# Kernel tuning notes

Hardware: AMD Instinct MI355X
Metric: run time of the kernel (lower is better)

The kernel has to match this reference:

```python
import jax, jax.numpy as jnp
import numpy as np

B, N, D, H, K, NH = 4096, 2048, 1024, 4096, 5, 8
HD = D // NH  # head dim


def setup_inputs() -> dict:
    key = jax.random.key(0)
    ks = jax.random.split(key, 12)
    s_d = np.float32(1.0 / np.sqrt(D))
    s_h = np.float32(1.0 / np.sqrt(H))
    rn = lambda k, sh, s: jax.random.normal(k, sh, dtype=jnp.float32) * s
    return {
        "morph0": jax.random.normal(ks[0], (B, D), dtype=jnp.float32),
        "stored_morph0": jax.random.normal(ks[1], (N, D), dtype=jnp.float32),
        "stored_morph1": jax.random.normal(ks[2], (N, D), dtype=jnp.float32),
        "wq": rn(ks[3], (D, D), s_d), "bq": jnp.zeros((D,), jnp.float32),
        "wk": rn(ks[4], (D, D), s_d), "bk": jnp.zeros((D,), jnp.float32),
        "wv": rn(ks[5], (D, D), s_d), "bv": jnp.zeros((D,), jnp.float32),
        "wo": rn(ks[6], (D, D), s_d), "bo": jnp.zeros((D,), jnp.float32),
        "w1": rn(ks[7], (H, D), s_d), "b1": jnp.zeros((H,), jnp.float32),
        "w2": rn(ks[8], (H, H), s_h), "b2": jnp.zeros((H,), jnp.float32),
        "w3": rn(ks[9], (D, H), s_h), "b3": jnp.zeros((D,), jnp.float32),
    }


def _l2norm(x):
    # F.normalize(dim=1): x / max(||x||, eps)
    n = jnp.sqrt(jnp.sum(x * x, axis=-1, keepdims=True))
    return x / jnp.maximum(n, 1e-12)


def reference(morph0, stored_morph0, stored_morph1,
              wq, bq, wk, bk, wv, bv, wo, bo,
              w1, b1, w2, b2, w3, b3):
    # ---- retrieve similar patterns: cosine sim + topk + fused gather-subtract ----
    qn = _l2norm(morph0)                       # [B, D]
    sn = _l2norm(stored_morph0)                # [N, D]
    sim = qn @ sn.T                            # [B, N]
    _, top_idx = jax.lax.top_k(sim, K)         # [B, K]
    evo = stored_morph1 - stored_morph0        # [N, D]
    selected = jnp.take(evo, top_idx, axis=0)  # [B, K, D] evolution vectors

    # ---- torch.nn.MultiheadAttention(D, 8, batch_first=True), eval mode ----
    q = (morph0 @ wq.T + bq).reshape(B, 1, NH, HD)      # [B, 1, NH, HD]
    k = (selected @ wk.T + bk).reshape(B, K, NH, HD)    # [B, K, NH, HD]
    v = (selected @ wv.T + bv).reshape(B, K, NH, HD)
    scores = jnp.einsum('bqhd,bkhd->bhqk', q, k) / np.float32(np.sqrt(HD))  # [B, NH, 1, K]
    attn = jax.nn.softmax(scores, axis=-1)
    ctx = jnp.einsum('bhqk,bkhd->bqhd', attn, v).reshape(B, 1, D)
    context = (ctx @ wo.T + bo)[:, 0, :]                # [B, D]
    attn_weights = attn.mean(axis=1)                    # [B, 1, K] (avg over heads)

    # ---- evolution net (dropout inactive in eval) + residual ----
    x = morph0 + context
    h1 = jax.nn.relu(x @ w1.T + b1)
    h2 = jax.nn.relu(h1 @ w2.T + b2)
    predicted = morph0 + (h2 @ w3.T + b3)
    return predicted, attn_weights
```

## Files before the change

### kernel.cpp

```cpp
#include <hip/hip_runtime.h>
#include <hip/hip_bf16.h>
#include <math.h>

typedef __bf16 bf16_t;
typedef __bf16 bf16x4 __attribute__((ext_vector_type(4)));
typedef __bf16 bf16x8 __attribute__((ext_vector_type(8)));
typedef float  f32x4  __attribute__((ext_vector_type(4)));

#define BB 4096
#define NN 2048
#define DD 1024
#define HH 4096
#define KSEL 5
#define NHEAD 8

__device__ __forceinline__ unsigned short bfbits(float f) {
  return __builtin_bit_cast(unsigned short, (bf16_t)f);
}

__device__ __forceinline__ void gload_lds16(const void* g, void* l) {
  __builtin_amdgcn_global_load_lds(
      (const __attribute__((address_space(1))) void*)g,
      (__attribute__((address_space(3))) void*)l, 16, 0, 0);
}

__device__ __forceinline__ ushort4 cvt4(float4 x) {
  ushort4 o;
  o.x = bfbits(x.x); o.y = bfbits(x.y); o.z = bfbits(x.z); o.w = bfbits(x.w);
  return o;
}

#define P_M0   1048576
#define P_S0   1572864
#define P_EVO  2097152
#define P_WQ   2359296
#define P_WKV  2883584
#define P_WO   3145728
#define P_W1   4194304
#define P_W2   8388608
#define P_W3   9437184
#define P_BKV  9437696
__global__ void __launch_bounds__(256)
prep_k(const float4* __restrict__ m0, const float4* __restrict__ s0,
       const float4* __restrict__ s1,
       const float4* __restrict__ wq, const float4* __restrict__ wk,
       const float4* __restrict__ wv, const float4* __restrict__ wo,
       const float4* __restrict__ w1, const float4* __restrict__ w2,
       const float4* __restrict__ w3,
       const float4* __restrict__ bk, const float4* __restrict__ bv,
       ushort4* __restrict__ m0b, ushort4* __restrict__ s0b,
       ushort4* __restrict__ evo,
       ushort4* __restrict__ wqb, ushort4* __restrict__ wkvb,
       ushort4* __restrict__ wob,
       ushort4* __restrict__ w1b, ushort4* __restrict__ w2b,
       ushort4* __restrict__ w3b, float4* __restrict__ bkv)
{
  const int stride = gridDim.x * 256;
  for (int i = blockIdx.x * 256 + threadIdx.x; i < P_BKV; i += stride) {
    if (i < P_M0) {
      m0b[i] = cvt4(m0[i]);
    } else if (i < P_S0) {
      int j = i - P_M0; s0b[j] = cvt4(s0[j]);
    } else if (i < P_EVO) {
      int j = i - P_S0;
      float4 a = s0[j], b = s1[j];
      float4 d; d.x = b.x - a.x; d.y = b.y - a.y; d.z = b.z - a.z; d.w = b.w - a.w;
      evo[j] = cvt4(d);
    } else if (i < P_WQ) {
      int j = i - P_EVO; wqb[j] = cvt4(wq[j]);
    } else if (i < P_WKV) {
      int j = i - P_WQ;
      wkvb[j] = cvt4(j < 262144 ? wk[j] : wv[j - 262144]);
    } else if (i < P_WO) {
      int j = i - P_WKV; wob[j] = cvt4(wo[j]);
    } else if (i < P_W1) {
      int j = i - P_WO; w1b[j] = cvt4(w1[j]);
    } else if (i < P_W2) {
      int j = i - P_W1; w2b[j] = cvt4(w2[j]);
    } else if (i < P_W3) {
      int j = i - P_W2; w3b[j] = cvt4(w3[j]);
    } else {
      int j = i - P_W3;
      bkv[j] = (j < 256) ? bk[j] : bv[j - 256];
    }
  }
}

__global__ void rnormd_k(const float* __restrict__ s0, double* __restrict__ rnd) {
  __shared__ double red[256];
  int n = blockIdx.x, tid = threadIdx.x;
  const float4* row = (const float4*)(s0 + (size_t)n * DD);
  float4 x = row[tid];
  double ss = (double)x.x * x.x + (double)x.y * x.y + (double)x.z * x.z + (double)x.w * x.w;
  red[tid] = ss; __syncthreads();
  for (int s = 128; s > 0; s >>= 1) {
    if (tid < s) red[tid] += red[tid + s];
    __syncthreads();
  }
  if (tid == 0) rnd[n] = 1.0 / fmax(sqrt(red[0]), 1e-12);
}

template<bool RELU, bool RESID, bool OUTBF16>
__global__ void __launch_bounds__(256)
gemm_bt(const bf16_t* __restrict__ A, const bf16_t* __restrict__ Bw,
        const float* __restrict__ bias, const float* __restrict__ resid,
        float* __restrict__ outf, bf16_t* __restrict__ outb,
        int M, int Nn, int Kk)
{
  __shared__ alignas(16) bf16_t At[2][4096];
  __shared__ alignas(16) bf16_t Bt[2][4096];
  const int tid = threadIdx.x;
  const int wave = tid >> 6, lane = tid & 63;
  const int wm = wave >> 1, wn = wave & 1;
  const int bm = blockIdx.y << 7, bn = blockIdx.x << 7;
  const int ln15 = lane & 15, ln4 = lane >> 4;

  const int srow  = (wave << 4) + (lane >> 2);
  const int scolb = (((lane & 3) ^ ((lane >> 3) & 3)) << 4);
  const char* pA0 = (const char*)A  + (size_t)(bm + srow) * Kk * 2 + scolb;
  const char* pA1 = (const char*)A  + (size_t)(bm + srow + 64) * Kk * 2 + scolb;
  const char* pB0 = (const char*)Bw + (size_t)(bn + srow) * Kk * 2 + scolb;
  const char* pB1 = (const char*)Bw + (size_t)(bn + srow + 64) * Kk * 2 + scolb;

  f32x4 zero = {0.f, 0.f, 0.f, 0.f};
  f32x4 acc[4][4];
  #pragma unroll
  for (int i = 0; i < 4; ++i)
    #pragma unroll
    for (int j = 0; j < 4; ++j) acc[i][j] = zero;

  const int rslot = (ln4 ^ ((ln15 >> 1) & 3)) << 3;
  const int fAoff = ((wm << 6) + ln15) * 32 + rslot;
  const int fBoff = ((wn << 6) + ln15) * 32 + rslot;

  const int nt = Kk >> 5;
  {
    char* lA = (char*)At[0] + (wave << 10);
    char* lB = (char*)Bt[0] + (wave << 10);
    gload_lds16(pA0, lA);
    gload_lds16(pA1, lA + 4096);
    gload_lds16(pB0, lB);
    gload_lds16(pB1, lB + 4096);
  }
  __syncthreads();

  for (int t = 0; t < nt; ++t) {
    const int cur = t & 1;
    if (t + 1 < nt) {
      size_t kb = (size_t)(t + 1) << 6;
      char* lA = (char*)At[cur ^ 1] + (wave << 10);
      char* lB = (char*)Bt[cur ^ 1] + (wave << 10);
      gload_lds16(pA0 + kb, lA);
      gload_lds16(pA1 + kb, lA + 4096);
      gload_lds16(pB0 + kb, lB);
      gload_lds16(pB1 + kb, lB + 4096);
    }
    bf16x8 av[4], bv[4];
    #pragma unroll
    for (int i = 0; i < 4; ++i) av[i] = *(const bf16x8*)(&At[cur][fAoff + i * 512]);
    #pragma unroll
    for (int j = 0; j < 4; ++j) bv[j] = *(const bf16x8*)(&Bt[cur][fBoff + j * 512]);
    #pragma unroll
    for (int i = 0; i < 4; ++i)
      #pragma unroll
      for (int j = 0; j < 4; ++j)
        acc[i][j] = __builtin_amdgcn_mfma_f32_16x16x32_bf16(av[i], bv[j], acc[i][j], 0, 0, 0);
    __syncthreads();
  }

  const int r0 = bm + (wm << 6) + ((lane >> 4) << 2);
  const int c0 = bn + (wn << 6) + ln15;
  #pragma unroll
  for (int i = 0; i < 4; ++i) {
    #pragma unroll
    for (int j = 0; j < 4; ++j) {
      #pragma unroll
      for (int r = 0; r < 4; ++r) {
        int row = r0 + i * 16 + r;
        int col = c0 + j * 16;
        size_t o = (size_t)row * Nn + col;
        float v = acc[i][j][r];
        if (bias)  v += bias[col];
        if (RESID) v += resid[o];
        if (RELU)  v = fmaxf(v, 0.f);
        if (OUTBF16) outb[o] = (bf16_t)v;
        else         outf[o] = v;
      }
    }
  }
}

template<bool RELU>
__global__ void __launch_bounds__(512, 4)
gemm_hp(const bf16_t* __restrict__ A, const bf16_t* __restrict__ Bw,
        const float* __restrict__ bias, bf16_t* __restrict__ outb,
        int Nn, int Kk, int nbx)
{
  __shared__ alignas(16) bf16_t As[2][4096];
  __shared__ alignas(16) bf16_t Bs[2][8192];
  const int tid  = threadIdx.x;
  const int lane = tid & 63, wv = tid >> 6;
  const int wm = wv >> 2, wn = wv & 3;
  const int ln15 = lane & 15, ln4 = lane >> 4;

  const int nwg = gridDim.x;
  const int q = nwg >> 3, r = nwg & 7;
  const int xcd = blockIdx.x & 7, loc = blockIdx.x >> 3;
  const int swz = (xcd < r ? xcd * (q + 1) : r * (q + 1) + (xcd - r) * q) + loc;
  const int bm = (swz / nbx) << 7;
  const int bn = (swz % nbx) << 8;

  const int NT = Kk >> 5;

  f32x4 acc[4][4];
  f32x4 zero = {0.f, 0.f, 0.f, 0.f};
  #pragma unroll
  for (int i = 0; i < 4; ++i)
    #pragma unroll
    for (int j = 0; j < 4; ++j) acc[i][j] = zero;

  const int sslot = (lane & 3) ^ ((lane >> 3) & 3);
  auto stageA = [&](bf16_t* lds, int kt) {
    int row = wv * 16 + (lane >> 2);
    gload_lds16(A + (size_t)(bm + row) * Kk + kt * 32 + sslot * 8,
                (char*)lds + wv * 1024);
  };
  auto stageB = [&](bf16_t* lds, int kt) {
    #pragma unroll
    for (int u = 0; u < 2; ++u) {
      int rowbase = u * 128 + wv * 16;
      int row = rowbase + (lane >> 2);
      gload_lds16(Bw + (size_t)(bn + row) * Kk + kt * 32 + sslot * 8,
                  (char*)lds + rowbase * 64);
    }
  };

  stageA(As[0], 0); stageB(Bs[0], 0);
  asm volatile("s_waitcnt vmcnt(0)" ::: "memory");
  __builtin_amdgcn_s_barrier();
  __builtin_amdgcn_sched_barrier(0);

  const int rslot = (ln4 ^ ((ln15 >> 1) & 3)) << 4;

  for (int t = 0; t < NT; ++t) {
    const int cur = t & 1;
    const char* Ab = (const char*)As[cur];
    const char* Bb = (const char*)Bs[cur];
    const bool more = (t + 1 < NT);
    bf16x8 av[4], bv[4];

    #pragma unroll
    for (int mi = 0; mi < 4; ++mi) {
      const int row = wm * 64 + mi * 16 + ln15;
      av[mi] = *(const bf16x8*)(Ab + row * 64 + rslot);
    }
    #pragma unroll
    for (int nj = 0; nj < 4; ++nj) {
      const int row = wn * 64 + nj * 16 + ln15;
      bv[nj] = *(const bf16x8*)(Bb + row * 64 + rslot);
    }
    if (more) { stageA(As[cur ^ 1], t + 1); stageB(Bs[cur ^ 1], t + 1); }

    __builtin_amdgcn_s_setprio(1);
    #pragma unroll
    for (int mi = 0; mi < 4; ++mi)
      #pragma unroll
      for (int nj = 0; nj < 4; ++nj)
        acc[mi][nj] = __builtin_amdgcn_mfma_f32_16x16x32_bf16(
            av[mi], bv[nj], acc[mi][nj], 0, 0, 0);
    __builtin_amdgcn_s_setprio(0);

    asm volatile("s_waitcnt vmcnt(0)" ::: "memory");
    __builtin_amdgcn_sched_barrier(0);
    __builtin_amdgcn_s_barrier();
    __builtin_amdgcn_sched_barrier(0);
  }

  #pragma unroll
  for (int am = 0; am < 4; ++am) {
    #pragma unroll
    for (int an = 0; an < 4; ++an) {
      #pragma unroll
      for (int rr = 0; rr < 4; ++rr) {
        int row = bm + wm * 64 + am * 16 + (lane >> 4) * 4 + rr;
        int col = bn + wn * 64 + an * 16 + ln15;
        float v = acc[am][an][rr] + bias[col];
        if (RELU) v = fmaxf(v, 0.f);
        outb[(size_t)row * Nn + col] = (bf16_t)v;
      }
    }
  }
}

__global__ void __launch_bounds__(256)
topk8_k(const float* __restrict__ sim, const double* __restrict__ rnd,
        int* __restrict__ cand)
{
  __shared__ float vals[NN];
  __shared__ float rv[256];
  __shared__ int   ri[256];
  int b = blockIdx.x, tid = threadIdx.x;
  for (int t = 0; t < NN / 256; ++t) {
    int i = tid + t * 256;
    vals[i] = sim[(size_t)b * NN + i] * (float)rnd[i];
  }
  __syncthreads();
  for (int p = 0; p < 8; ++p) {
    float bvv = -INFINITY; int bi = NN;
    for (int t = 0; t < NN / 256; ++t) {
      int i = tid + t * 256;
      float v = vals[i];
      if (v > bvv) { bvv = v; bi = i; }
    }
    rv[tid] = bvv; ri[tid] = bi;
    __syncthreads();
    for (int s = 128; s > 0; s >>= 1) {
      if (tid < s) {
        float v2 = rv[tid + s]; int i2 = ri[tid + s];
        if (v2 > rv[tid] || (v2 == rv[tid] && i2 < ri[tid])) { rv[tid] = v2; ri[tid] = i2; }
      }
      __syncthreads();
    }
    if (tid == 0) {
      int wsel = ri[0];
      cand[b * 8 + p] = wsel;
      vals[wsel] = -INFINITY;
    }
    __syncthreads();
  }
}

__global__ void __launch_bounds__(256)
refine_k(const float* __restrict__ m0, const float* __restrict__ s0,
         const double* __restrict__ rnd, const int* __restrict__ cand,
         int* __restrict__ topidx)
{
  __shared__ double red[256];
  __shared__ double vals[8];
  int b = blockIdx.x, tid = threadIdx.x;
  int cs[8];
  #pragma unroll
  for (int j = 0; j < 8; ++j) cs[j] = cand[b * 8 + j];
  const float* q = m0 + (size_t)b * DD;
  double part[8];
  #pragma unroll
  for (int j = 0; j < 8; ++j) part[j] = 0.0;
  for (int d = tid; d < DD; d += 256) {
    double qd = (double)q[d];
    #pragma unroll
    for (int j = 0; j < 8; ++j)
      part[j] += qd * (double)s0[(size_t)cs[j] * DD + d];
  }
  for (int j = 0; j < 8; ++j) {
    red[tid] = part[j]; __syncthreads();
    for (int s = 128; s > 0; s >>= 1) {
      if (tid < s) red[tid] += red[tid + s];
      __syncthreads();
    }
    if (tid == 0) vals[j] = red[0] * rnd[cs[j]];
    __syncthreads();
  }
  if (tid == 0) {
    bool used[8] = {false,false,false,false,false,false,false,false};
    for (int p = 0; p < KSEL; ++p) {
      int best = -1;
      for (int j = 0; j < 8; ++j) {
        if (used[j]) continue;
        if (best < 0 || vals[j] > vals[best] ||
            (vals[j] == vals[best] && cs[j] < cs[best])) best = j;
      }
      used[best] = true;
      topidx[b * KSEL + p] = cs[best];
    }
  }
}

__global__ void __launch_bounds__(256)
attn_k(const bf16_t* __restrict__ q, const bf16_t* __restrict__ eKV,
       const int* __restrict__ tidx,
       bf16_t* __restrict__ ctx, float* __restrict__ attn_out)
{
  __shared__ float aw[NHEAD][KSEL];
  const int b = blockIdx.x, t = threadIdx.x;
  const int d0 = t << 2;
  int idx[KSEL];
  #pragma unroll
  for (int j = 0; j < KSEL; ++j) idx[j] = tidx[b * KSEL + j];

  bf16x4 qv = *(const bf16x4*)(q + (size_t)b * DD + d0);
  float s[KSEL];
  #pragma unroll
  for (int j = 0; j < KSEL; ++j) {
    bf16x4 kv = *(const bf16x4*)(eKV + (size_t)idx[j] * 2048 + d0);
    float p = (float)qv[0] * (float)kv[0] + (float)qv[1] * (float)kv[1]
            + (float)qv[2] * (float)kv[2] + (float)qv[3] * (float)kv[3];
    #pragma unroll
    for (int m = 16; m > 0; m >>= 1) p += __shfl_xor(p, m);
    s[j] = p * 0.08838834764831845f;
  }
  float mx = s[0];
  #pragma unroll
  for (int j = 1; j < KSEL; ++j) mx = fmaxf(mx, s[j]);
  float e[KSEL], sum = 0.f;
  #pragma unroll
  for (int j = 0; j < KSEL; ++j) { e[j] = expf(s[j] - mx); sum += e[j]; }
  float inv = 1.f / sum;

  float c0 = 0.f, c1 = 0.f, c2 = 0.f, c3 = 0.f;
  #pragma unroll
  for (int j = 0; j < KSEL; ++j) {
    float a = e[j] * inv;
    bf16x4 vv = *(const bf16x4*)(eKV + (size_t)idx[j] * 2048 + 1024 + d0);
    c0 += a * (float)vv[0]; c1 += a * (float)vv[1];
    c2 += a * (float)vv[2]; c3 += a * (float)vv[3];
    if ((t & 31) == 0) aw[t >> 5][j] = a;
  }
  bf16x4 co; co[0] = (bf16_t)c0; co[1] = (bf16_t)c1; co[2] = (bf16_t)c2; co[3] = (bf16_t)c3;
  *(bf16x4*)(ctx + (size_t)b * DD + d0) = co;
  __syncthreads();
  if (t < KSEL) {
    float m = 0.f;
    #pragma unroll
    for (int hh = 0; hh < NHEAD; ++hh) m += aw[hh][t];
    attn_out[(size_t)b * KSEL + t] = m * 0.125f;
  }
}

extern "C" void kernel_launch(void* const* d_in, const int* in_sizes, int n_in,
                              void* d_out, int out_size, void* d_ws, size_t ws_size,
                              hipStream_t stream) {
  (void)in_sizes; (void)n_in; (void)out_size; (void)ws_size;
  const float* morph0 = (const float*)d_in[0];
  const float* s0     = (const float*)d_in[1];
  const float* s1     = (const float*)d_in[2];
  const float* wq = (const float*)d_in[3];  const float* bq = (const float*)d_in[4];
  const float* wk = (const float*)d_in[5];  const float* bk = (const float*)d_in[6];
  const float* wv = (const float*)d_in[7];  const float* bv = (const float*)d_in[8];
  const float* wo = (const float*)d_in[9];  const float* bo = (const float*)d_in[10];
  const float* w1 = (const float*)d_in[11]; const float* b1 = (const float*)d_in[12];
  const float* w2 = (const float*)d_in[13]; const float* b2 = (const float*)d_in[14];
  const float* w3 = (const float*)d_in[15]; const float* b3 = (const float*)d_in[16];

  char* ws = (char*)d_ws;
  size_t off = 0;
  auto alloc = [&](size_t bytes) { char* p = ws + off; off += (bytes + 255) & ~(size_t)255; return p; };

  float*  sim  = (float*) alloc((size_t)BB * NN * 4);
  bf16_t* m0b  = (bf16_t*)alloc((size_t)BB * DD * 2);
  bf16_t* s0b  = (bf16_t*)alloc((size_t)NN * DD * 2);
  bf16_t* evo  = (bf16_t*)alloc((size_t)NN * DD * 2);
  double* rnd  = (double*)alloc((size_t)NN * 8);
  int*    cand = (int*)   alloc((size_t)BB * 8 * 4);
  int*    tidx = (int*)   alloc((size_t)BB * KSEL * 4);
  bf16_t* qb   = (bf16_t*)alloc((size_t)BB * DD * 2);
  bf16_t* eKVb = (bf16_t*)alloc((size_t)NN * 2048 * 2);
  bf16_t* ctxb = (bf16_t*)alloc((size_t)BB * DD * 2);
  bf16_t* xb   = (bf16_t*)alloc((size_t)BB * DD * 2);
  bf16_t* wqb  = (bf16_t*)alloc((size_t)DD * DD * 2);
  bf16_t* wkvb = (bf16_t*)alloc((size_t)2048 * DD * 2);
  bf16_t* wob  = (bf16_t*)alloc((size_t)DD * DD * 2);
  bf16_t* w1b  = (bf16_t*)alloc((size_t)HH * DD * 2);
  bf16_t* w2b  = (bf16_t*)alloc((size_t)HH * HH * 2);
  bf16_t* w3b  = (bf16_t*)alloc((size_t)DD * HH * 2);
  float*  bkv  = (float*) alloc((size_t)2048 * 4);
  bf16_t* h2b  = (bf16_t*)alloc((size_t)BB * HH * 2);
  bf16_t* h1b  = (bf16_t*)sim;
  float*  attn_out = (float*)d_out + (size_t)BB * DD;

  prep_k<<<dim3(2048), dim3(256), 0, stream>>>(
      (const float4*)morph0, (const float4*)s0, (const float4*)s1,
      (const float4*)wq, (const float4*)wk, (const float4*)wv, (const float4*)wo,
      (const float4*)w1, (const float4*)w2, (const float4*)w3,
      (const float4*)bk, (const float4*)bv,
      (ushort4*)m0b, (ushort4*)s0b, (ushort4*)evo,
      (ushort4*)wqb, (ushort4*)wkvb, (ushort4*)wob,
      (ushort4*)w1b, (ushort4*)w2b, (ushort4*)w3b, (float4*)bkv);
  rnormd_k<<<dim3(NN), dim3(256), 0, stream>>>(s0, rnd);

  gemm_bt<false,false,false><<<dim3(NN/128, BB/128), dim3(256), 0, stream>>>(
      m0b, s0b, nullptr, nullptr, sim, nullptr, BB, NN, DD);
  topk8_k<<<dim3(BB), dim3(256), 0, stream>>>(sim, rnd, cand);
  refine_k<<<dim3(BB), dim3(256), 0, stream>>>(morph0, s0, rnd, cand, tidx);

  gemm_bt<false,false,true><<<dim3(DD/128, BB/128), dim3(256), 0, stream>>>(
      m0b, wqb, bq, nullptr, nullptr, qb, BB, DD, DD);
  gemm_bt<false,false,true><<<dim3(2048/128, NN/128), dim3(256), 0, stream>>>(
      evo, wkvb, bkv, nullptr, nullptr, eKVb, NN, 2048, DD);

  attn_k<<<dim3(BB), dim3(256), 0, stream>>>(qb, eKVb, tidx, ctxb, attn_out);

  gemm_bt<false,true,true><<<dim3(DD/128, BB/128), dim3(256), 0, stream>>>(
      ctxb, wob, bo, morph0, nullptr, xb, BB, DD, DD);

  gemm_hp<true><<<dim3((BB/128)*(HH/256)), dim3(512), 0, stream>>>(
      xb, w1b, b1, h1b, HH, DD, HH/256);
  gemm_hp<true><<<dim3((BB/128)*(HH/256)), dim3(512), 0, stream>>>(
      h1b, w2b, b2, h2b, HH, HH, HH/256);
  gemm_bt<false,true,false><<<dim3(DD/128, BB/128), dim3(256), 0, stream>>>(
      h2b, w3b, b3, morph0, (float*)d_out, nullptr, BB, DD, HH);
}
```

Baseline: 525.9 us.

## Use 256x256 eight-wave GEMM with split-phase LDS pipeline; fuse small kernels

Replaces the 128x256 MLP GEMM with a 256x256 tile kernel. It uses a K-step of 64, double-buffered half-tiles and an interleaved read/stage/MFMA schedule with partial vmcnt waits, which raises arithmetic intensity per LDS load and hides global latency. The row-norm kernel is folded into the prep kernel as extra blocks, and top-k is merged with the fp64 refine step, which removes two launches and the candidate buffer round trip. The larger tile raises register and LDS pressure, halves the workgroup count and drops occupancy to 2 blocks per CU.

Result: faster. 506.7 us (-3.7%).

```diff
diff --git a/kernel.cpp b/kernel.cpp
--- a/kernel.cpp
+++ b/kernel.cpp
@@ -53,10 +53,25 @@
        ushort4* __restrict__ wqb, ushort4* __restrict__ wkvb,
        ushort4* __restrict__ wob,
        ushort4* __restrict__ w1b, ushort4* __restrict__ w2b,
-       ushort4* __restrict__ w3b, float4* __restrict__ bkv)
+       ushort4* __restrict__ w3b, float4* __restrict__ bkv,
+       double* __restrict__ rnd)
 {
-  const int stride = gridDim.x * 256;
-  for (int i = blockIdx.x * 256 + threadIdx.x; i < P_BKV; i += stride) {
+  __shared__ double red[256];
+  const int tid = threadIdx.x;
+  if (blockIdx.x >= 2048) {
+    int n = blockIdx.x - 2048;
+    float4 x = s0[(size_t)n * 256 + tid];
+    double ss = (double)x.x * x.x + (double)x.y * x.y + (double)x.z * x.z + (double)x.w * x.w;
+    red[tid] = ss; __syncthreads();
+    for (int s = 128; s > 0; s >>= 1) {
+      if (tid < s) red[tid] += red[tid + s];
+      __syncthreads();
+    }
+    if (tid == 0) rnd[n] = 1.0 / fmax(sqrt(red[0]), 1e-12);
+    return;
+  }
+  const int stride = 2048 * 256;
+  for (int i = blockIdx.x * 256 + tid; i < P_BKV; i += stride) {
     if (i < P_M0) {
       m0b[i] = cvt4(m0[i]);
     } else if (i < P_S0) {
@@ -86,20 +101,6 @@
   }
 }
 
-__global__ void rnormd_k(const float* __restrict__ s0, double* __restrict__ rnd) {
-  __shared__ double red[256];
-  int n = blockIdx.x, tid = threadIdx.x;
-  const float4* row = (const float4*)(s0 + (size_t)n * DD);
-  float4 x = row[tid];
-  double ss = (double)x.x * x.x + (double)x.y * x.y + (double)x.z * x.z + (double)x.w * x.w;
-  red[tid] = ss; __syncthreads();
-  for (int s = 128; s > 0; s >>= 1) {
-    if (tid < s) red[tid] += red[tid + s];
-    __syncthreads();
-  }
-  if (tid == 0) rnd[n] = 1.0 / fmax(sqrt(red[0]), 1e-12);
-}
-
 template<bool RELU, bool RESID, bool OUTBF16>
 __global__ void __launch_bounds__(256)
 gemm_bt(const bf16_t* __restrict__ A, const bf16_t* __restrict__ Bw,
@@ -191,15 +192,14 @@
 }
 
 template<bool RELU>
-__global__ void __launch_bounds__(512, 4)
-gemm_hp(const bf16_t* __restrict__ A, const bf16_t* __restrict__ Bw,
-        const float* __restrict__ bias, bf16_t* __restrict__ outb,
-        int Nn, int Kk, int nbx)
+__global__ void __launch_bounds__(512, 2)
+gemm8(const bf16_t* __restrict__ A, const bf16_t* __restrict__ Bw,
+      const float* __restrict__ bias, bf16_t* __restrict__ outb,
+      int Nn, int Kk, int nbx)
 {
-  __shared__ alignas(16) bf16_t As[2][4096];
-  __shared__ alignas(16) bf16_t Bs[2][8192];
-  const int tid  = threadIdx.x;
-  const int lane = tid & 63, wv = tid >> 6;
+  __shared__ alignas(16) bf16_t As[2][2][8192];
+  __shared__ alignas(16) bf16_t Bs[2][2][8192];
+  const int lane = threadIdx.x & 63, wv = threadIdx.x >> 6;
   const int wm = wv >> 2, wn = wv & 3;
   const int ln15 = lane & 15, ln4 = lane >> 4;
 
@@ -207,83 +207,123 @@
   const int q = nwg >> 3, r = nwg & 7;
   const int xcd = blockIdx.x & 7, loc = blockIdx.x >> 3;
   const int swz = (xcd < r ? xcd * (q + 1) : r * (q + 1) + (xcd - r) * q) + loc;
-  const int bm = (swz / nbx) << 7;
+  const int bm = (swz / nbx) << 8;
   const int bn = (swz % nbx) << 8;
 
-  const int NT = Kk >> 5;
-
-  f32x4 acc[4][4];
+  const int NT = Kk >> 6;
+
+  f32x4 acc[8][4];
   f32x4 zero = {0.f, 0.f, 0.f, 0.f};
   #pragma unroll
-  for (int i = 0; i < 4; ++i)
+  for (int i = 0; i < 8; ++i)
     #pragma unroll
     for (int j = 0; j < 4; ++j) acc[i][j] = zero;
 
-  const int sslot = (lane & 3) ^ ((lane >> 3) & 3);
-  auto stageA = [&](bf16_t* lds, int kt) {
-    int row = wv * 16 + (lane >> 2);
-    gload_lds16(A + (size_t)(bm + row) * Kk + kt * 32 + sslot * 8,
-                (char*)lds + wv * 1024);
+  auto stA = [&](int mh, int buf, int kt) {
+    #pragma unroll
+    for (int u = 0; u < 2; ++u) {
+      int lr = u * 64 + wv * 8 + (lane >> 3);
+      int gr = ((lr >> 6) << 7) | (mh << 6) | (lr & 63);
+      int slot = (lane & 7) ^ (lr & 7);
+      gload_lds16(A + (size_t)(bm + gr) * Kk + kt * 64 + slot * 8,
+                  (char*)&As[buf][mh][0] + (u * 64 + wv * 8) * 128);
+    }
   };
-  auto stageB = [&](bf16_t* lds, int kt) {
+  auto stB = [&](int nh, int buf, int kt) {
     #pragma unroll
     for (int u = 0; u < 2; ++u) {
-      int rowbase = u * 128 + wv * 16;
-      int row = rowbase + (lane >> 2);
-      gload_lds16(Bw + (size_t)(bn + row) * Kk + kt * 32 + sslot * 8,
-                  (char*)lds + rowbase * 64);
+      int lr = u * 64 + wv * 8 + (lane >> 3);
+      int gr = ((lr >> 5) << 6) | (nh << 5) | (lr & 31);
+      int slot = (lane & 7) ^ (lr & 7);
+      gload_lds16(Bw + (size_t)(bn + gr) * Kk + kt * 64 + slot * 8,
+                  (char*)&Bs[buf][nh][0] + (u * 64 + wv * 8) * 128);
     }
   };
 
-  stageA(As[0], 0); stageB(Bs[0], 0);
-  asm volatile("s_waitcnt vmcnt(0)" ::: "memory");
+  stB(0, 0, 0); stA(1, 0, 0); stB(1, 0, 0); stA(0, 0, 0);
+  stB(0, 1, 1); stA(1, 1, 1); stB(1, 1, 1);
+  asm volatile("s_waitcnt vmcnt(6)" ::: "memory");
   __builtin_amdgcn_s_barrier();
-  __builtin_amdgcn_sched_barrier(0);
-
-  const int rslot = (ln4 ^ ((ln15 >> 1) & 3)) << 4;
-
-  for (int t = 0; t < NT; ++t) {
-    const int cur = t & 1;
-    const char* Ab = (const char*)As[cur];
-    const char* Bb = (const char*)Bs[cur];
-    const bool more = (t + 1 < NT);
-    bf16x8 av[4], bv[4];
-
-    #pragma unroll
-    for (int mi = 0; mi < 4; ++mi) {
-      const int row = wm * 64 + mi * 16 + ln15;
-      av[mi] = *(const bf16x8*)(Ab + row * 64 + rslot);
-    }
-    #pragma unroll
-    for (int nj = 0; nj < 4; ++nj) {
-      const int row = wn * 64 + nj * 16 + ln15;
-      bv[nj] = *(const bf16x8*)(Bb + row * 64 + rslot);
-    }
-    if (more) { stageA(As[cur ^ 1], t + 1); stageB(Bs[cur ^ 1], t + 1); }
-
-    __builtin_amdgcn_s_setprio(1);
-    #pragma unroll
-    for (int mi = 0; mi < 4; ++mi)
-      #pragma unroll
-      for (int nj = 0; nj < 4; ++nj)
-        acc[mi][nj] = __builtin_amdgcn_mfma_f32_16x16x32_bf16(
-            av[mi], bv[nj], acc[mi][nj], 0, 0, 0);
-    __builtin_amdgcn_s_setprio(0);
-
-    asm volatile("s_waitcnt vmcnt(0)" ::: "memory");
+
+#define RD_A(MH, BF)                                                              \
+    _Pragma("unroll") for (int mi = 0; mi < 4; ++mi)                              \
+      _Pragma("unroll") for (int kk = 0; kk < 2; ++kk) {                          \
+        const int lr = wm * 64 + mi * 16 + ln15;                                  \
+        avv[mi][kk] = *(const bf16x8*)((const char*)&As[BF][MH][0] + lr * 128 +   \
+                                       ((((kk << 2) | ln4) ^ (ln15 & 7)) << 4));  \
+      }
+#define RD_B(NH, BF)                                                              \
+    _Pragma("unroll") for (int nj = 0; nj < 2; ++nj)                              \
+      _Pragma("unroll") for (int kk = 0; kk < 2; ++kk) {                          \
+        const int lr = wn * 32 + nj * 16 + ln15;                                  \
+        bvv[nj][kk] = *(const bf16x8*)((const char*)&Bs[BF][NH][0] + lr * 128 +   \
+                                       ((((kk << 2) | ln4) ^ (ln15 & 7)) << 4));  \
+      }
+#define GATE                                                                      \
+    __builtin_amdgcn_s_barrier();                                                 \
+    asm volatile("s_waitcnt lgkmcnt(0)" ::: "memory");                            \
     __builtin_amdgcn_sched_barrier(0);
+#define MMA(MH, NH)                                                               \
+    __builtin_amdgcn_s_setprio(1);                                                \
+    _Pragma("unroll") for (int kk = 0; kk < 2; ++kk)                              \
+      _Pragma("unroll") for (int mi = 0; mi < 4; ++mi)                            \
+        _Pragma("unroll") for (int nj = 0; nj < 2; ++nj)                          \
+          acc[(MH)*4+mi][(NH)*2+nj] = __builtin_amdgcn_mfma_f32_16x16x32_bf16(    \
+              avv[mi][kk], bvv[nj][kk], acc[(MH)*4+mi][(NH)*2+nj], 0, 0, 0);      \
+    __builtin_amdgcn_s_setprio(0);                                                \
     __builtin_amdgcn_s_barrier();
-    __builtin_amdgcn_sched_barrier(0);
-  }
-
-  #pragma unroll
-  for (int am = 0; am < 4; ++am) {
+
+  for (int base = 0; base < NT; base += 2) {
+    const bool more = (base + 2 < NT);
+    bf16x8 avv[4][2], bvv[2][2];
+
+    RD_A(0, 0); RD_B(0, 0);
+    stA(0, 1, base + 1);
+    asm volatile("s_waitcnt lgkmcnt(8)");
+    GATE; MMA(0, 0);
+    RD_A(1, 0);
+    if (more) stB(0, 0, base + 2);
+    GATE; MMA(1, 0);
+    RD_B(1, 0);
+    if (more) stA(1, 0, base + 2);
+    GATE; MMA(1, 1);
+    RD_A(0, 0);
+    if (more) {
+      stB(1, 0, base + 2);
+      asm volatile("s_waitcnt vmcnt(6)" ::: "memory");
+    } else {
+      asm volatile("s_waitcnt vmcnt(0)" ::: "memory");
+    }
+    GATE; MMA(0, 1);
+
+    RD_A(0, 1); RD_B(0, 1);
+    if (more) stA(0, 0, base + 2);
+    asm volatile("s_waitcnt lgkmcnt(8)");
+    GATE; MMA(0, 0);
+    RD_A(1, 1);
+    if (more) stB(0, 1, base + 3);
+    GATE; MMA(1, 0);
+    RD_B(1, 1);
+    if (more) stA(1, 1, base + 3);
+    GATE; MMA(1, 1);
+    RD_A(0, 1);
+    if (more) stB(1, 1, base + 3);
+    asm volatile("s_waitcnt vmcnt(6)" ::: "memory");
+    GATE; MMA(0, 1);
+  }
+#undef RD_A
+#undef RD_B
+#undef GATE
+#undef MMA
+
+  #pragma unroll
+  for (int am = 0; am < 8; ++am) {
     #pragma unroll
     for (int an = 0; an < 4; ++an) {
       #pragma unroll
       for (int rr = 0; rr < 4; ++rr) {
-        int row = bm + wm * 64 + am * 16 + (lane >> 4) * 4 + rr;
-        int col = bn + wn * 64 + an * 16 + ln15;
+        int row = bm + wm * 128 + (am >> 2) * 64 + (am & 3) * 16 + (lane >> 4) * 4 + rr;
+        int col = bn + wn * 64 + (an >> 1) * 32 + (an & 1) * 16 + ln15;
         float v = acc[am][an][rr] + bias[col];
         if (RELU) v = fmaxf(v, 0.f);
         outb[(size_t)row * Nn + col] = (bf16_t)v;
@@ -293,13 +333,17 @@
 }
 
 __global__ void __launch_bounds__(256)
-topk8_k(const float* __restrict__ sim, const double* __restrict__ rnd,
-        int* __restrict__ cand)
+topk_refine_k(const float* __restrict__ sim, const double* __restrict__ rnd,
+              const float* __restrict__ m0, const float* __restrict__ s0,
+              int* __restrict__ topidx)
 {
   __shared__ float vals[NN];
   __shared__ float rv[256];
   __shared__ int   ri[256];
-  int b = blockIdx.x, tid = threadIdx.x;
+  __shared__ int   c8[8];
+  __shared__ double dred[256];
+  __shared__ double dvals[8];
+  const int b = blockIdx.x, tid = threadIdx.x;
   for (int t = 0; t < NN / 256; ++t) {
     int i = tid + t * 256;
     vals[i] = sim[(size_t)b * NN + i] * (float)rnd[i];
@@ -323,41 +367,31 @@
     }
     if (tid == 0) {
       int wsel = ri[0];
-      cand[b * 8 + p] = wsel;
+      c8[p] = wsel;
       vals[wsel] = -INFINITY;
     }
     __syncthreads();
   }
-}
-
-__global__ void __launch_bounds__(256)
-refine_k(const float* __restrict__ m0, const float* __restrict__ s0,
-         const double* __restrict__ rnd, const int* __restrict__ cand,
-         int* __restrict__ topidx)
-{
-  __shared__ double red[256];
-  __shared__ double vals[8];
-  int b = blockIdx.x, tid = threadIdx.x;
   int cs[8];
   #pragma unroll
-  for (int j = 0; j < 8; ++j) cs[j] = cand[b * 8 + j];
-  const float* q = m0 + (size_t)b * DD;
+  for (int j = 0; j < 8; ++j) cs[j] = c8[j];
+  const float* qrow = m0 + (size_t)b * DD;
   double part[8];
   #pragma unroll
   for (int j = 0; j < 8; ++j) part[j] = 0.0;
   for (int d = tid; d < DD; d += 256) {
-    double qd = (double)q[d];
+    double qd = (double)qrow[d];
     #pragma unroll
     for (int j = 0; j < 8; ++j)
       part[j] += qd * (double)s0[(size_t)cs[j] * DD + d];
   }
   for (int j = 0; j < 8; ++j) {
-    red[tid] = part[j]; __syncthreads();
+    dred[tid] = part[j]; __syncthreads();
     for (int s = 128; s > 0; s >>= 1) {
-      if (tid < s) red[tid] += red[tid + s];
+      if (tid < s) dred[tid] += dred[tid + s];
       __syncthreads();
     }
-    if (tid == 0) vals[j] = red[0] * rnd[cs[j]];
+    if (tid == 0) dvals[j] = dred[0] * rnd[cs[j]];
     __syncthreads();
   }
   if (tid == 0) {
@@ -366,8 +400,8 @@
       int best = -1;
       for (int j = 0; j < 8; ++j) {
         if (used[j]) continue;
-        if (best < 0 || vals[j] > vals[best] ||
-            (vals[j] == vals[best] && cs[j] < cs[best])) best = j;
+        if (best < 0 || dvals[j] > dvals[best] ||
+            (dvals[j] == dvals[best] && cs[j] < cs[best])) best = j;
       }
       used[best] = true;
       topidx[b * KSEL + p] = cs[best];
@@ -450,7 +484,6 @@
   bf16_t* s0b  = (bf16_t*)alloc((size_t)NN * DD * 2);
   bf16_t* evo  = (bf16_t*)alloc((size_t)NN * DD * 2);
   double* rnd  = (double*)alloc((size_t)NN * 8);
-  int*    cand = (int*)   alloc((size_t)BB * 8 * 4);
   int*    tidx = (int*)   alloc((size_t)BB * KSEL * 4);
   bf16_t* qb   = (bf16_t*)alloc((size_t)BB * DD * 2);
   bf16_t* eKVb = (bf16_t*)alloc((size_t)NN * 2048 * 2);
@@ -467,20 +500,18 @@
   bf16_t* h1b  = (bf16_t*)sim;
   float*  attn_out = (float*)d_out + (size_t)BB * DD;
 
-  prep_k<<<dim3(2048), dim3(256), 0, stream>>>(
+  prep_k<<<dim3(4096), dim3(256), 0, stream>>>(
       (const float4*)morph0, (const float4*)s0, (const float4*)s1,
       (const float4*)wq, (const float4*)wk, (const float4*)wv, (const float4*)wo,
       (const float4*)w1, (const float4*)w2, (const float4*)w3,
       (const float4*)bk, (const float4*)bv,
       (ushort4*)m0b, (ushort4*)s0b, (ushort4*)evo,
       (ushort4*)wqb, (ushort4*)wkvb, (ushort4*)wob,
-      (ushort4*)w1b, (ushort4*)w2b, (ushort4*)w3b, (float4*)bkv);
-  rnormd_k<<<dim3(NN), dim3(256), 0, stream>>>(s0, rnd);
+      (ushort4*)w1b, (ushort4*)w2b, (ushort4*)w3b, (float4*)bkv, rnd);
 
   gemm_bt<false,false,false><<<dim3(NN/128, BB/128), dim3(256), 0, stream>>>(
       m0b, s0b, nullptr, nullptr, sim, nullptr, BB, NN, DD);
-  topk8_k<<<dim3(BB), dim3(256), 0, stream>>>(sim, rnd, cand);
-  refine_k<<<dim3(BB), dim3(256), 0, stream>>>(morph0, s0, rnd, cand, tidx);
+  topk_refine_k<<<dim3(BB), dim3(256), 0, stream>>>(sim, rnd, morph0, s0, tidx);
 
   gemm_bt<false,false,true><<<dim3(DD/128, BB/128), dim3(256), 0, stream>>>(
       m0b, wqb, bq, nullptr, nullptr, qb, BB, DD, DD);
@@ -492,9 +523,9 @@
   gemm_bt<false,true,true><<<dim3(DD/128, BB/128), dim3(256), 0, stream>>>(
       ctxb, wob, bo, morph0, nullptr, xb, BB, DD, DD);
 
-  gemm_hp<true><<<dim3((BB/128)*(HH/256)), dim3(512), 0, stream>>>(
+  gemm8<true><<<dim3((BB/256)*(HH/256)), dim3(512), 0, stream>>>(
       xb, w1b, b1, h1b, HH, DD, HH/256);
-  gemm_hp<true><<<dim3((BB/128)*(HH/256)), dim3(512), 0, stream>>>(
+  gemm8<true><<<dim3((BB/256)*(HH/256)), dim3(512), 0, stream>>>(
       h1b, w2b, b2, h2b, HH, HH, HH/256);
   gemm_bt<false,true,false><<<dim3(DD/128, BB/128), dim3(256), 0, stream>>>(
       h2b, w3b, b3, morph0, (float*)d_out, nullptr, BB, DD, HH);
```
